# Optimization experiments

Measured on AMD Instinct MI355X. Metric: run time of the kernel, lower is better.

## Reference

```python
import math
import jax, jax.numpy as jnp
import numpy as np

S = 64.0
M = 0.5
C = 1.5
K = 16
EPS = 1e-6
IN = 128
OUT = 10000
B = 1024


def _l2norm(x, axis):
    # matches torch.nn.functional.normalize (eps=1e-12)
    n = jnp.linalg.norm(x, axis=axis, keepdims=True)
    return x / jnp.maximum(n, 1e-12)


def setup_inputs() -> dict:
    key = jax.random.key(0)
    k1, k2, k3, k4 = jax.random.split(key, 4)
    inp = jax.random.normal(k1, (B, IN), dtype=jnp.float32)
    factor = jax.random.uniform(k2, (B, 1), dtype=jnp.float32)
    label = jax.random.randint(k3, (B,), 0, OUT)
    # xavier_uniform over (k, in, out): fan_in=IN, fan_out=OUT (last two dims)
    limit = math.sqrt(6.0 / (IN + OUT))
    weight = jax.random.uniform(k4, (K, IN, OUT), dtype=jnp.float32, minval=-limit, maxval=limit)
    return {"input": inp, "factor": factor, "label": label, "weight": weight}


def reference(input, factor, label, weight):
    # disguise-adaptive margin: (B,1)
    func_a = jnp.power(C, factor / 12.0) * M
    threshold = math.pi - func_a  # (B,1)

    xn = _l2norm(input, axis=1)          # (B, IN)
    wn = _l2norm(weight, axis=1)         # (K, IN, OUT), normalized along IN

    # batched sub-center matmul then max over sub-centers k
    cos_all = jnp.einsum('bf,kfo->kbo', xn, wn)   # (K, B, OUT)
    cos_theta = jnp.max(cos_all, axis=0)          # (B, OUT)

    theta = jnp.arccos(jnp.clip(cos_theta, -1.0 + EPS, 1.0 - EPS))
    one_hot = jax.nn.one_hot(label, OUT, dtype=theta.dtype)  # (B, OUT)
    selected = jnp.where(theta > threshold, jnp.zeros_like(one_hot), one_hot)
    logits = jnp.cos(jnp.where(selected.astype(bool), theta + func_a, theta)) * S

    # cross-entropy (mean reduction)
    logp = jax.nn.log_softmax(logits, axis=-1)
    cls_loss = -jnp.mean(jnp.take_along_axis(logp, label[:, None], axis=1))

    # top-1 accuracy (percent), detached stat
    pred = jnp.argmax(logits, axis=1)
    prec1 = jnp.mean((pred == label).astype(jnp.float32)) * 100.0
    return cls_loss, prec1
```

## Files before the change

kernel.cpp:

```cpp
#include <hip/hip_runtime.h>
#include <hip/hip_bf16.h>
#include <math.h>

#define BB    1024
#define FIN   128
#define NOUT  10000
#define NBLK  79
#define NCB   158
#define NK    16
#define NPART (NCB * 2)
#define LDX   136

typedef __attribute__((ext_vector_type(8))) short short8;
typedef __attribute__((ext_vector_type(4))) float floatx4;

__device__ __forceinline__ unsigned packbf(float a, float b) {
    __hip_bfloat162 h = __float22bfloat162_rn(make_float2(a, b));
    union { __hip_bfloat162 h2; unsigned u; } v;
    v.h2 = h;
    return v.u;
}

__device__ __forceinline__ unsigned scale2(unsigned p, float wi) {
    float lo = __uint_as_float(p << 16) * wi;
    float hi = __uint_as_float(p & 0xffff0000u) * wi;
    return packbf(lo, hi);
}

__device__ __forceinline__ void async16(const void* g, void* l) {
    __builtin_amdgcn_global_load_lds(
        (const __attribute__((address_space(1))) unsigned int*)g,
        (__attribute__((address_space(3))) unsigned int*)l, 16, 0, 0);
}

__global__ void rowprep(const float* __restrict__ X, const float* __restrict__ factor,
                        float* __restrict__ xinv, float* __restrict__ fa_out,
                        float* __restrict__ thr_out) {
    int b = blockIdx.x;
    int lane = threadIdx.x;
    float v0 = X[b * FIN + lane];
    float v1 = X[b * FIN + 64 + lane];
    float s = v0 * v0 + v1 * v1;
    #pragma unroll
    for (int off = 32; off > 0; off >>= 1) s += __shfl_down(s, off);
    if (lane == 0) {
        xinv[b] = 1.0f / fmaxf(sqrtf(s), 1e-12f);
        float fa = powf(1.5f, factor[b] * (1.0f / 12.0f)) * 0.5f;
        fa_out[b] = fa;
        thr_out[b] = (float)M_PI - fa;
    }
}

__global__ __launch_bounds__(256) void wconv(
    const float* __restrict__ W, unsigned char* __restrict__ Wbf,
    const float* __restrict__ X, const float* __restrict__ factor,
    float* __restrict__ xinv, float* __restrict__ fa_out, float* __restrict__ thr_out) {

    __shared__ float s[64 * 64];
    __shared__ uint4 wout[1024];
    __shared__ float sq2[256];
    __shared__ float wis[64];

    const int tid = threadIdx.x;

    if (blockIdx.x >= NK * NCB) {
        int rb = blockIdx.x - NK * NCB;
        int w4 = tid >> 6, lane = tid & 63;
        for (int i = w4; i < 64; i += 4) {
            int row = rb * 64 + i;
            float v0 = X[row * FIN + lane];
            float v1 = X[row * FIN + 64 + lane];
            float ss = v0 * v0 + v1 * v1;
            #pragma unroll
            for (int off = 32; off > 0; off >>= 1) ss += __shfl_down(ss, off);
            if (lane == 0) {
                xinv[row] = 1.0f / fmaxf(sqrtf(ss), 1e-12f);
                float fa = powf(1.5f, factor[row] * (1.0f / 12.0f)) * 0.5f;
                fa_out[row] = fa;
                thr_out[row] = (float)M_PI - fa;
            }
        }
        return;
    }

    const int k  = blockIdx.x / NCB;
    const int cb = blockIdx.x - k * NCB;
    const int o0 = cb * 64;
    const int col = tid & 63, seg = tid >> 6;
    const int c   = tid >> 2, sub = tid & 3;
    const int wn_ = c >> 5, n2_ = (c >> 4) & 1, l15_ = c & 15;

    float sqacc = 0.0f;
    #pragma unroll
    for (int h = 0; h < 2; h++) {
        #pragma unroll
        for (int it = 0; it < 4; it++) {
            int idx = it * 256 + tid;
            int f = idx >> 4, c4 = idx & 15;
            int o = o0 + c4 * 4;
            float4 v = make_float4(0.f, 0.f, 0.f, 0.f);
            if (o < NOUT)
                v = *(const float4*)(W + (size_t)(k * FIN + h * 64 + f) * NOUT + o);
            *(float4*)(s + f * 64 + c4 * 4) = v;
        }
        __syncthreads();
        float ss = 0.0f;
        #pragma unroll
        for (int f2 = 0; f2 < 16; f2++) {
            float x = s[(seg * 16 + f2) * 64 + col];
            ss = fmaf(x, x, ss);
        }
        sqacc += ss;
        #pragma unroll
        for (int i = 0; i < 2; i++) {
            int tcl = sub * 2 + i;
            int tcg = h * 8 + tcl;
            int kk = tcg >> 2, qq = tcg & 3;
            int fb = tcl * 8;
            uint4 u;
            u.x = packbf(s[(fb + 0) * 64 + c], s[(fb + 1) * 64 + c]);
            u.y = packbf(s[(fb + 2) * 64 + c], s[(fb + 3) * 64 + c]);
            u.z = packbf(s[(fb + 4) * 64 + c], s[(fb + 5) * 64 + c]);
            u.w = packbf(s[(fb + 6) * 64 + c], s[(fb + 7) * 64 + c]);
            wout[wn_ * 512 + n2_ * 256 + kk * 64 + qq * 16 + l15_] = u;
        }
        __syncthreads();
    }
    sq2[tid] = sqacc;
    __syncthreads();
    if (tid < 64)
        wis[tid] = 1.0f / fmaxf(sqrtf(sq2[tid] + sq2[tid + 64] + sq2[tid + 128] + sq2[tid + 192]), 1e-12f);
    __syncthreads();

    unsigned char* dst = Wbf + ((size_t)k * NCB + cb) * 16384;
    #pragma unroll
    for (int i = 0; i < 4; i++) {
        int idx = i * 256 + tid;
        int ccol = ((idx >> 9) << 5) + (((idx >> 8) & 1) << 4) + (idx & 15);
        float wi = wis[ccol];
        uint4 u = wout[idx];
        uint4 r;
        r.x = scale2(u.x, wi);
        r.y = scale2(u.y, wi);
        r.z = scale2(u.z, wi);
        r.w = scale2(u.w, wi);
        *(uint4*)(dst + (size_t)idx * 16) = r;
    }
}

__global__ __launch_bounds__(512, 2) void gemm_mx(
    const float* __restrict__ X, const unsigned char* __restrict__ Wbf,
    const int* __restrict__ label, const float* __restrict__ xinv,
    float2* __restrict__ partial, float* __restrict__ cosl) {

    __shared__ union {
        short xs[128 * LDX];
        short bb[2][8192];
    } u;

    const int tid  = threadIdx.x;
    const int lane = tid & 63;
    const int w    = tid >> 6;
    const int l15  = lane & 15;
    const int q    = lane >> 4;
    const int wm   = w & 3;
    const int wn   = w >> 2;

    const int id    = blockIdx.x;
    const int group = id >> 6;
    const int sub   = id & 63;
    const int cb    = group * 8 + (sub & 7);
    const int y     = sub >> 3;
    if (cb >= NCB) return;
    const int r0 = y * 128;
    const int o0 = cb * 64;

    #pragma unroll
    for (int it = 0; it < 8; it++) {
        int idx = it * 512 + tid;
        int row = idx >> 5;
        int c4  = idx & 31;
        const float4 v = *(const float4*)(X + (size_t)(r0 + row) * FIN + c4 * 4);
        float xi = xinv[r0 + row];
        uint2 p;
        p.x = packbf(v.x * xi, v.y * xi);
        p.y = packbf(v.z * xi, v.w * xi);
        *(uint2*)(u.xs + row * LDX + c4 * 4) = p;
    }
    __syncthreads();

    short8 af[2][4];
    #pragma unroll
    for (int mt = 0; mt < 2; mt++)
        #pragma unroll
        for (int kk = 0; kk < 4; kk++)
            af[mt][kk] = *(const short8*)(u.xs + (wm * 32 + mt * 16 + l15) * LDX + kk * 32 + q * 8);
    __syncthreads();

    auto issue = [&](int k) {
        const unsigned char* g = Wbf + ((size_t)k * NCB + cb) * 16384
                                 + (size_t)w * 2048 + (size_t)lane * 16;
        short* d = u.bb[k & 1] + w * 1024;
        async16(g, d);
        async16(g + 1024, d + 512);
    };

    issue(0);

    floatx4 maxv[2][2];
    #pragma unroll
    for (int mt = 0; mt < 2; mt++)
        #pragma unroll
        for (int n2 = 0; n2 < 2; n2++)
            #pragma unroll
            for (int r = 0; r < 4; r++)
                maxv[mt][n2][r] = -INFINITY;

    for (int k = 0; k < NK; k++) {
        __syncthreads();
        if (k < NK - 1) issue(k + 1);
        const short* wt = u.bb[k & 1];

        floatx4 acc[2][2];
        #pragma unroll
        for (int mt = 0; mt < 2; mt++)
            #pragma unroll
            for (int n2 = 0; n2 < 2; n2++)
                acc[mt][n2] = (floatx4){0.f, 0.f, 0.f, 0.f};
        #pragma unroll
        for (int kk = 0; kk < 4; kk++) {
            short8 bf[2];
            #pragma unroll
            for (int n2 = 0; n2 < 2; n2++)
                bf[n2] = *(const short8*)(wt + wn * 4096 + n2 * 2048 + kk * 512 + lane * 8);
            #pragma unroll
            for (int mt = 0; mt < 2; mt++)
                #pragma unroll
                for (int n2 = 0; n2 < 2; n2++)
                    acc[mt][n2] = __builtin_amdgcn_mfma_f32_16x16x32_bf16(
                        af[mt][kk], bf[n2], acc[mt][n2], 0, 0, 0);
        }
        #pragma unroll
        for (int mt = 0; mt < 2; mt++)
            #pragma unroll
            for (int n2 = 0; n2 < 2; n2++)
                #pragma unroll
                for (int r = 0; r < 4; r++)
                    maxv[mt][n2][r] = fmaxf(maxv[mt][n2][r], acc[mt][n2][r]);
    }

    #pragma unroll
    for (int mt = 0; mt < 2; mt++) {
        #pragma unroll
        for (int rr = 0; rr < 4; rr++) {
            int row = r0 + wm * 32 + mt * 16 + q * 4 + rr;
            int lb = label[row];
            float m = -1e30f, sum = 0.f;
            #pragma unroll
            for (int n2 = 0; n2 < 2; n2++) {
                int o = o0 + wn * 32 + n2 * 16 + l15;
                if (o < NOUT) {
                    float cc = maxv[mt][n2][rr];
                    if (o == lb) {
                        cosl[row] = cc;
                    } else {
                        float l = 64.0f * fminf(fmaxf(cc, -1.0f + 1e-6f), 1.0f - 1e-6f);
                        sum += __expf(l - 64.0f);
                        m = fmaxf(m, l);
                    }
                }
            }
            #pragma unroll
            for (int off = 1; off <= 8; off <<= 1) {
                sum += __shfl_xor(sum, off);
                m = fmaxf(m, __shfl_xor(m, off));
            }
            if (l15 == 0)
                partial[(size_t)row * NPART + cb * 2 + wn] = make_float2(m, sum);
        }
    }
}

__global__ __launch_bounds__(256, 2) void gemm_stats(
    const float* __restrict__ X, const float* __restrict__ W,
    const int* __restrict__ label, const float* __restrict__ xinv,
    float2* __restrict__ partial, float* __restrict__ cosl) {

    __shared__ short xs[128 * LDX];
    __shared__ short wt[128 * LDX];
    __shared__ float sqs[128][2];

    const int tid  = threadIdx.x;
    const int lane = tid & 63;
    const int w    = tid >> 6;
    const int l15  = lane & 15;
    const int q    = lane >> 4;
    const int wm   = w & 1;
    const int wn   = w >> 1;

    const int id    = blockIdx.x;
    const int group = id >> 6;
    const int sub   = id & 63;
    const int jb    = group * 8 + (sub & 7);
    const int y     = sub >> 3;
    if (jb >= NBLK) return;
    const int r0 = y * 128;
    const int o0 = jb * 128;

    #pragma unroll
    for (int it = 0; it < 16; it++) {
        int idx = it * 256 + tid;
        int row = idx >> 5;
        int c4  = idx & 31;
        const float4 v = *(const float4*)(X + (size_t)(r0 + row) * FIN + c4 * 4);
        uint2 p;
        p.x = packbf(v.x, v.y);
        p.y = packbf(v.z, v.w);
        *(uint2*)(xs + row * LDX + c4 * 4) = p;
    }

    const int st_o = (w & 1) * 64 + lane;
    const int st_f = (w >> 1) * 64;
    const int st_h = w >> 1;
    const int go   = o0 + st_o;
    const bool ov  = go < NOUT;

    float rw[64];
    {
        const float* Wp = W + (size_t)st_f * NOUT + go;
        #pragma unroll
        for (int g = 0; g < 16; g++)
            #pragma unroll
            for (int cc = 0; cc < 4; cc++)
                rw[g * 4 + cc] = ov ? Wp[(size_t)(g * 4 + cc) * NOUT] : 0.0f;
    }
    __syncthreads();

    short8 af[4][4];
    #pragma unroll
    for (int mt = 0; mt < 4; mt++)
        #pragma unroll
        for (int kk = 0; kk < 4; kk++)
            af[mt][kk] = *(const short8*)(xs + (wm * 64 + mt * 16 + l15) * LDX + kk * 32 + q * 8);

    floatx4 maxv[4][4];
    #pragma unroll
    for (int mt = 0; mt < 4; mt++)
        #pragma unroll
        for (int nt = 0; nt < 4; nt++)
            #pragma unroll
            for (int r = 0; r < 4; r++)
                maxv[mt][nt][r] = -INFINITY;

    for (int k = 0; k < NK; k++) {
        float sq = 0.0f;
        uint2 pk[16];
        #pragma unroll
        for (int g = 0; g < 16; g++) {
            float a0 = rw[g * 4 + 0], a1 = rw[g * 4 + 1];
            float a2 = rw[g * 4 + 2], a3 = rw[g * 4 + 3];
            sq = fmaf(a0, a0, sq); sq = fmaf(a1, a1, sq);
            sq = fmaf(a2, a2, sq); sq = fmaf(a3, a3, sq);
            pk[g].x = packbf(a0, a1);
            pk[g].y = packbf(a2, a3);
        }
        __syncthreads();
        #pragma unroll
        for (int g = 0; g < 16; g++)
            *(uint2*)(wt + st_o * LDX + st_f + g * 4) = pk[g];
        sqs[st_o][st_h] = sq;
        __syncthreads();

        if (k < NK - 1) {
            const float* Wn = W + ((size_t)(k + 1) * FIN + st_f) * NOUT + go;
            #pragma unroll
            for (int g = 0; g < 16; g++)
                #pragma unroll
                for (int cc = 0; cc < 4; cc++)
                    rw[g * 4 + cc] = ov ? Wn[(size_t)(g * 4 + cc) * NOUT] : 0.0f;
        }

        float wv[4];
        #pragma unroll
        for (int nt = 0; nt < 4; nt++) {
            int colx = wn * 64 + nt * 16 + l15;
            wv[nt] = 1.0f / fmaxf(sqrtf(sqs[colx][0] + sqs[colx][1]), 1e-12f);
        }

        #pragma unroll
        for (int h = 0; h < 2; h++) {
            floatx4 acc[4][2];
            #pragma unroll
            for (int mt = 0; mt < 4; mt++) {
                acc[mt][0] = (floatx4){0.f, 0.f, 0.f, 0.f};
                acc[mt][1] = (floatx4){0.f, 0.f, 0.f, 0.f};
            }
            #pragma unroll
            for (int kk = 0; kk < 4; kk++) {
                short8 bf0 = *(const short8*)(wt + (wn * 64 + (h * 2 + 0) * 16 + l15) * LDX + kk * 32 + q * 8);
                short8 bf1 = *(const short8*)(wt + (wn * 64 + (h * 2 + 1) * 16 + l15) * LDX + kk * 32 + q * 8);
                #pragma unroll
                for (int mt = 0; mt < 4; mt++) {
                    acc[mt][0] = __builtin_amdgcn_mfma_f32_16x16x32_bf16(af[mt][kk], bf0, acc[mt][0], 0, 0, 0);
                    acc[mt][1] = __builtin_amdgcn_mfma_f32_16x16x32_bf16(af[mt][kk], bf1, acc[mt][1], 0, 0, 0);
                }
            }
            #pragma unroll
            for (int mt = 0; mt < 4; mt++)
                #pragma unroll
                for (int n2 = 0; n2 < 2; n2++)
                    #pragma unroll
                    for (int r = 0; r < 4; r++)
                        maxv[mt][h * 2 + n2][r] =
                            fmaxf(maxv[mt][h * 2 + n2][r], acc[mt][n2][r] * wv[h * 2 + n2]);
        }
    }

    #pragma unroll
    for (int mt = 0; mt < 4; mt++) {
        #pragma unroll
        for (int rr = 0; rr < 4; rr++) {
            int row = r0 + wm * 64 + mt * 16 + q * 4 + rr;
            float xi = xinv[row];
            int lb = label[row];
            float m = -1e30f, sum = 0.f;
            #pragma unroll
            for (int nt = 0; nt < 4; nt++) {
                int o = o0 + wn * 64 + nt * 16 + l15;
                if (o < NOUT) {
                    float cc = maxv[mt][nt][rr] * xi;
                    if (o == lb) {
                        cosl[row] = cc;
                    } else {
                        float l = 64.0f * fminf(fmaxf(cc, -1.0f + 1e-6f), 1.0f - 1e-6f);
                        sum += __expf(l - 64.0f);
                        m = fmaxf(m, l);
                    }
                }
            }
            #pragma unroll
            for (int off = 1; off <= 8; off <<= 1) {
                sum += __shfl_xor(sum, off);
                m = fmaxf(m, __shfl_xor(m, off));
            }
            if (l15 == 0) {
                partial[(size_t)row * NPART + jb * 4 + wn * 2 + 0] = make_float2(m, sum);
                partial[(size_t)row * NPART + jb * 4 + wn * 2 + 1] = make_float2(-1e30f, 0.f);
            }
        }
    }
}

__global__ void finalize_rows(const float2* __restrict__ partial, const float* __restrict__ cosl,
                              const float* __restrict__ fa, const float* __restrict__ thr,
                              float2* __restrict__ rowres, int np) {
    int w = threadIdx.x >> 6;
    int lane = threadIdx.x & 63;
    int b = blockIdx.x * 4 + w;
    float m = -1e30f, s = 0.0f;
    for (int j = lane; j < np; j += 64) {
        float2 p = partial[(size_t)b * np + j];
        s += p.y;
        m = fmaxf(m, p.x);
    }
    #pragma unroll
    for (int off = 1; off < 64; off <<= 1) {
        s += __shfl_xor(s, off);
        m = fmaxf(m, __shfl_xor(m, off));
    }
    if (lane == 0) {
        float c = fminf(fmaxf(cosl[b], -1.0f + 1e-6f), 1.0f - 1e-6f);
        float theta = acosf(c);
        float ll = (theta > thr[b]) ? 64.0f * c : 64.0f * cosf(theta + fa[b]);
        float S = s + __expf(ll - 64.0f);
        float loss = 64.0f + logf(S) - ll;
        rowres[b] = make_float2(loss, (ll > m) ? 100.0f : 0.0f);
    }
}

__global__ void finalize_sum(const float2* __restrict__ rowres, float* __restrict__ out) {
    __shared__ float sl[1024];
    __shared__ float sc[1024];
    int b = threadIdx.x;
    float2 v = rowres[b];
    sl[b] = v.x;
    sc[b] = v.y;
    __syncthreads();
    for (int st = 512; st > 0; st >>= 1) {
        if (b < st) { sl[b] += sl[b + st]; sc[b] += sc[b + st]; }
        __syncthreads();
    }
    if (b == 0) {
        out[0] = sl[0] * (1.0f / 1024.0f);
        out[1] = sc[0] * (1.0f / 1024.0f);
    }
}

extern "C" void kernel_launch(void* const* d_in, const int* in_sizes, int n_in,
                              void* d_out, int out_size, void* d_ws, size_t ws_size,
                              hipStream_t stream) {
    const float* X      = (const float*)d_in[0];
    const float* factor = (const float*)d_in[1];
    const int*   label  = (const int*)d_in[2];
    const float* W      = (const float*)d_in[3];
    float* out = (float*)d_out;
    float* ws  = (float*)d_ws;

    float*  xinv = ws;
    float*  fa   = ws + 1024;
    float*  thr  = ws + 2048;
    float*  cosl = ws + 3072;
    float2* rowres = (float2*)(ws + 4096);
    float2* partial = (float2*)(ws + 6144);
    unsigned char* Wbf = (unsigned char*)d_ws + 4 * 1024 * 1024;

    const size_t wbf_bytes = (size_t)NK * NCB * 16384;
    const size_t need = 4ull * 1024 * 1024 + wbf_bytes;

    if (ws_size >= need) {
        wconv<<<NK * NCB + 16, 256, 0, stream>>>(W, Wbf, X, factor, xinv, fa, thr);
        gemm_mx<<<1280, 512, 0, stream>>>(X, Wbf, label, xinv, partial, cosl);
    } else {
        rowprep<<<BB, 64, 0, stream>>>(X, factor, xinv, fa, thr);
        gemm_stats<<<640, 256, 0, stream>>>(X, W, label, xinv, partial, cosl);
    }
    finalize_rows<<<BB / 4, 256, 0, stream>>>(partial, cosl, fa, thr, rowres, NPART);
    finalize_sum<<<1, BB, 0, stream>>>(rowres, out);
}
```

Measured before the change: 205.4 us.

## Triple-buffer weight tiles in GEMM and async-load weight conversion input

The GEMM kernel goes from a double-buffered to a triple-buffered LDS ring for the bf16 weight tiles. It prefetches two sub-centers ahead and uses explicit vmcnt waits plus a raw s_barrier in place of __syncthreads, so global loads overlap more with MFMA work. The weight-conversion kernel now issues async global-to-LDS loads for both feature halves up front, with the out-of-range columns clamped to column 0 instead of zero-filled, and waits per half with vmcnt. This costs more LDS in the GEMM, which may lower occupancy, and relies on hand-counted wait counts being correct.

```diff
diff --git a/kernel.cpp b/kernel.cpp
--- a/kernel.cpp
+++ b/kernel.cpp
@@ -56,7 +56,7 @@
     const float* __restrict__ X, const float* __restrict__ factor,
     float* __restrict__ xinv, float* __restrict__ fa_out, float* __restrict__ thr_out) {
 
-    __shared__ float s[64 * 64];
+    __shared__ __attribute__((aligned(16))) float s[2][64 * 64];
     __shared__ uint4 wout[1024];
     __shared__ float sq2[256];
     __shared__ float wis[64];
@@ -89,8 +89,8 @@
     const int col = tid & 63, seg = tid >> 6;
     const int c   = tid >> 2, sub = tid & 3;
     const int wn_ = c >> 5, n2_ = (c >> 4) & 1, l15_ = c & 15;
-
-    float sqacc = 0.0f;
+    const int w   = tid >> 6;
+
     #pragma unroll
     for (int h = 0; h < 2; h++) {
         #pragma unroll
@@ -98,16 +98,27 @@
             int idx = it * 256 + tid;
             int f = idx >> 4, c4 = idx & 15;
             int o = o0 + c4 * 4;
-            float4 v = make_float4(0.f, 0.f, 0.f, 0.f);
-            if (o < NOUT)
-                v = *(const float4*)(W + (size_t)(k * FIN + h * 64 + f) * NOUT + o);
-            *(float4*)(s + f * 64 + c4 * 4) = v;
-        }
-        __syncthreads();
+            if (o >= NOUT) o = 0;
+            float* dst = &s[h][(it * 256 + w * 64) * 4];
+            async16(W + (size_t)(k * FIN + h * 64 + f) * NOUT + o, dst);
+        }
+    }
+
+    float sqacc = 0.0f;
+    #pragma unroll
+    for (int h = 0; h < 2; h++) {
+        if (h == 0) {
+            asm volatile("s_waitcnt vmcnt(4)" ::: "memory");
+        } else {
+            asm volatile("s_waitcnt vmcnt(0)" ::: "memory");
+        }
+        __builtin_amdgcn_s_barrier();
+        __builtin_amdgcn_sched_barrier(0);
+
         float ss = 0.0f;
         #pragma unroll
         for (int f2 = 0; f2 < 16; f2++) {
-            float x = s[(seg * 16 + f2) * 64 + col];
+            float x = s[h][(seg * 16 + f2) * 64 + col];
             ss = fmaf(x, x, ss);
         }
         sqacc += ss;
@@ -118,13 +129,12 @@
             int kk = tcg >> 2, qq = tcg & 3;
             int fb = tcl * 8;
             uint4 u;
-            u.x = packbf(s[(fb + 0) * 64 + c], s[(fb + 1) * 64 + c]);
-            u.y = packbf(s[(fb + 2) * 64 + c], s[(fb + 3) * 64 + c]);
-            u.z = packbf(s[(fb + 4) * 64 + c], s[(fb + 5) * 64 + c]);
-            u.w = packbf(s[(fb + 6) * 64 + c], s[(fb + 7) * 64 + c]);
+            u.x = packbf(s[h][(fb + 0) * 64 + c], s[h][(fb + 1) * 64 + c]);
+            u.y = packbf(s[h][(fb + 2) * 64 + c], s[h][(fb + 3) * 64 + c]);
+            u.z = packbf(s[h][(fb + 4) * 64 + c], s[h][(fb + 5) * 64 + c]);
+            u.w = packbf(s[h][(fb + 6) * 64 + c], s[h][(fb + 7) * 64 + c]);
             wout[wn_ * 512 + n2_ * 256 + kk * 64 + qq * 16 + l15_] = u;
         }
-        __syncthreads();
     }
     sq2[tid] = sqacc;
     __syncthreads();
@@ -155,7 +165,7 @@
 
     __shared__ union {
         short xs[128 * LDX];
-        short bb[2][8192];
+        short bb[3][8192];
     } u;
 
     const int tid  = threadIdx.x;
@@ -197,15 +207,20 @@
             af[mt][kk] = *(const short8*)(u.xs + (wm * 32 + mt * 16 + l15) * LDX + kk * 32 + q * 8);
     __syncthreads();
 
-    auto issue = [&](int k) {
-        const unsigned char* g = Wbf + ((size_t)k * NCB + cb) * 16384
+    const unsigned char* gbase = Wbf + (size_t)cb * 16384
                                  + (size_t)w * 2048 + (size_t)lane * 16;
-        short* d = u.bb[k & 1] + w * 1024;
+    auto issue = [&](int k, int buf) {
+        const unsigned char* g = gbase + (size_t)k * ((size_t)NCB * 16384);
+        short* d = u.bb[buf] + w * 1024;
         async16(g, d);
         async16(g + 1024, d + 512);
     };
 
-    issue(0);
+    issue(0, 0);
+    issue(1, 1);
+
+    const int wboff = wn * 4096 + lane * 8;
+    const floatx4 z4 = {0.f, 0.f, 0.f, 0.f};
 
     floatx4 maxv[2][2];
     #pragma unroll
@@ -216,29 +231,36 @@
             for (int r = 0; r < 4; r++)
                 maxv[mt][n2][r] = -INFINITY;
 
+    #pragma unroll
     for (int k = 0; k < NK; k++) {
-        __syncthreads();
-        if (k < NK - 1) issue(k + 1);
-        const short* wt = u.bb[k & 1];
+        if (k == NK - 1) {
+            asm volatile("s_waitcnt vmcnt(0)" ::: "memory");
+        } else {
+            asm volatile("s_waitcnt vmcnt(2)" ::: "memory");
+        }
+        __builtin_amdgcn_s_barrier();
+        __builtin_amdgcn_sched_barrier(0);
+
+        if (k < NK - 2) issue(k + 2, (k + 2) % 3);
+
+        const short* wb = u.bb[k % 3] + wboff;
 
         floatx4 acc[2][2];
         #pragma unroll
-        for (int mt = 0; mt < 2; mt++)
-            #pragma unroll
-            for (int n2 = 0; n2 < 2; n2++)
-                acc[mt][n2] = (floatx4){0.f, 0.f, 0.f, 0.f};
-        #pragma unroll
         for (int kk = 0; kk < 4; kk++) {
-            short8 bf[2];
-            #pragma unroll
-            for (int n2 = 0; n2 < 2; n2++)
-                bf[n2] = *(const short8*)(wt + wn * 4096 + n2 * 2048 + kk * 512 + lane * 8);
-            #pragma unroll
-            for (int mt = 0; mt < 2; mt++)
-                #pragma unroll
-                for (int n2 = 0; n2 < 2; n2++)
-                    acc[mt][n2] = __builtin_amdgcn_mfma_f32_16x16x32_bf16(
-                        af[mt][kk], bf[n2], acc[mt][n2], 0, 0, 0);
+            short8 b0 = *(const short8*)(wb + kk * 512);
+            short8 b1 = *(const short8*)(wb + 2048 + kk * 512);
+            if (kk == 0) {
+                acc[0][0] = __builtin_amdgcn_mfma_f32_16x16x32_bf16(af[0][0], b0, z4, 0, 0, 0);
+                acc[0][1] = __builtin_amdgcn_mfma_f32_16x16x32_bf16(af[0][0], b1, z4, 0, 0, 0);
+                acc[1][0] = __builtin_amdgcn_mfma_f32_16x16x32_bf16(af[1][0], b0, z4, 0, 0, 0);
+                acc[1][1] = __builtin_amdgcn_mfma_f32_16x16x32_bf16(af[1][0], b1, z4, 0, 0, 0);
+            } else {
+                acc[0][0] = __builtin_amdgcn_mfma_f32_16x16x32_bf16(af[0][kk], b0, acc[0][0], 0, 0, 0);
+                acc[0][1] = __builtin_amdgcn_mfma_f32_16x16x32_bf16(af[0][kk], b1, acc[0][1], 0, 0, 0);
+                acc[1][0] = __builtin_amdgcn_mfma_f32_16x16x32_bf16(af[1][kk], b0, acc[1][0], 0, 0, 0);
+                acc[1][1] = __builtin_amdgcn_mfma_f32_16x16x32_bf16(af[1][kk], b1, acc[1][1], 0, 0, 0);
+            }
         }
         #pragma unroll
         for (int mt = 0; mt < 2; mt++)
```

New measurement: 249.8 us. 21.7% more time.
